# Kernel optimization log

Hardware: AMD Instinct MI355X
Metric: run time of the kernel (lower is better)

The kernel has to match this reference:

```python
import jax, jax.numpy as jnp
import numpy as np

NEG_SLOPE = 0.01  # LeakyReLU default
STRIDE = 5        # group_length // 4
EPS = 1e-5        # RMSNorm eps


def leaky_relu(x):
    return jnp.where(x >= 0, x, NEG_SLOPE * x)


def rmsnorm(x, w):
    return x * jax.lax.rsqrt(jnp.mean(x * x, axis=-1, keepdims=True) + EPS) * w


def s6(x, fc1_w, fc1_b, fc2_w, fc2_b, fc3_w, fc3_b, A):
    # x: [B, L, D] with D = 2*d_model; A: [D, N]
    delta = jax.nn.softplus(x @ fc1_w.T + fc1_b)        # [B, L, D]
    Bm = x @ fc2_w.T + fc2_b                             # [B, L, N]
    Cm = x @ fc3_w.T + fc3_b                             # [B, L, N]
    dA = jnp.exp(jnp.einsum('bld,dn->bldn', delta, A))   # [B, L, D, N]
    dBx = jnp.einsum('bld,bln,bld->bldn', delta, Bm, x)  # delta * B * x

    def step(h, inp):
        dA_t, dBx_t = inp
        h = dA_t * h + dBx_t
        return h, h

    B_, L, D, N = dA.shape
    h0 = jnp.zeros((B_, D, N), dtype=x.dtype)
    _, hs = jax.lax.scan(step, h0, (jnp.swapaxes(dA, 0, 1), jnp.swapaxes(dBx, 0, 1)))
    hs = jnp.swapaxes(hs, 0, 1)                          # [B, L, D, N]
    return jnp.einsum('bln,bldn->bld', Cm, hs)           # [B, L, D]


def setup_inputs() -> dict:
    key = jax.random.key(0)
    ks = iter(jax.random.split(key, 32))

    def rn(shape, scale=0.02):
        return scale * jax.random.normal(next(ks), shape, dtype=jnp.float32)

    B, band, gl, d, N, L = 256, 189, 20, 128, 128, 34
    di = 2 * d
    return {
        'x': jax.random.normal(next(ks), (B, 1, band), dtype=jnp.float32),
        'conv_w': rn((d, 1, gl)), 'conv_b': rn((d,)),
        'norm_w': jnp.ones((d,), jnp.float32),
        'inp_w': rn((di, d)), 'inp_b': rn((di,)),
        'seqconv_w': rn((L, L, 3)), 'seqconv_b': rn((L,)),
        'convlin_w': rn((di, di)), 'convlin_b': rn((di,)),
        'fc1_w': rn((di, di)), 'fc1_b': rn((di,)),
        'fc2_w': rn((N, di)), 'fc2_b': rn((N,)),
        'fc3_w': rn((N, di)), 'fc3_b': rn((N,)),
        'A': jnp.ones((di, N), jnp.float32) / jnp.sqrt(jnp.float32(N)),
        'D_w': rn((di, d)), 'D_b': rn((di,)),
        'out_w': rn((d, di)), 'out_b': rn((d,)),
        'fnn1_w': rn((64, L * d)), 'fnn1_b': rn((64,)),
        'fnn2_w': rn((32, 64)), 'fnn2_b': rn((32,)),
    }


def reference(x, conv_w, conv_b, norm_w, inp_w, inp_b, seqconv_w, seqconv_b,
              convlin_w, convlin_b, fc1_w, fc1_b, fc2_w, fc2_b, fc3_w, fc3_b,
              A, D_w, D_b, out_w, out_b, fnn1_w, fnn1_b, fnn2_w, fnn2_b):
    # group division: Conv1d(1, d, k=20, stride=5) + LeakyReLU
    g = jax.lax.conv_general_dilated(x, conv_w, (STRIDE,), [(0, 0)],
                                     dimension_numbers=('NCH', 'OIH', 'NCH'))
    g = leaky_relu(g + conv_b[None, :, None])            # [B, d, L]
    h = jnp.swapaxes(g, 1, 2)                            # [B, L, d]
    # Mamba block
    xn = rmsnorm(h, norm_w)
    xp = xn @ inp_w.T + inp_b                            # [B, L, 2d]
    # Conv1d(seq_len, seq_len, k=3, pad=1): seq axis L is the channel dim
    xc = jax.lax.conv_general_dilated(xp, seqconv_w, (1,), [(1, 1)],
                                      dimension_numbers=('NCH', 'OIH', 'NCH'))
    xc = jax.nn.silu(xc + seqconv_b[None, :, None])
    xc = xc @ convlin_w.T + convlin_b                    # [B, L, 2d]
    xs = s6(xc, fc1_w, fc1_b, fc2_w, fc2_b, fc3_w, fc3_b, A)
    y = jax.nn.silu(xs) * jax.nn.silu(xn @ D_w.T + D_b)  # gated
    y = y @ out_w.T + out_b                              # [B, L, d]
    # FNN head
    f = y.reshape(y.shape[0], -1)                        # [B, L*d]
    f = leaky_relu(f @ fnn1_w.T + fnn1_b)
    return f @ fnn2_w.T + fnn2_b                         # [B, 32]
```

## Files before the change

### kernel.cpp

```cpp
#include <hip/hip_runtime.h>
#include <math.h>


#define NB    256
#define LL    34
#define DD    128
#define DI    256
#define NN    128
#define MM    (NB*LL)

using u16 = unsigned short;
typedef __attribute__((ext_vector_type(8))) short short8;
typedef __attribute__((ext_vector_type(4))) float f32x4;

__device__ __forceinline__ float silu_f(float x)  { return x / (1.f + __expf(-x)); }
__device__ __forceinline__ float softplus_f(float x) {
    return fmaxf(x, 0.f) + __logf(1.f + __expf(-fabsf(x)));
}
__device__ __forceinline__ float leaky_f(float x) { return (x >= 0.f) ? x : 0.01f * x; }

__device__ __forceinline__ u16 f2bf(float x) {
    unsigned u = __float_as_uint(x);
    return (u16)((u + 0x7FFF + ((u >> 16) & 1)) >> 16);
}
__device__ __forceinline__ float bf2f(u16 h) {
    return __uint_as_float(((unsigned)h) << 16);
}
__device__ __forceinline__ void f2pair(float v, u16* h, u16* l) {
    u16 hh = f2bf(v);
    *h = hh;
    *l = f2bf(v - bf2f(hh));
}

__global__ __launch_bounds__(256)
void prep_all_k(const float* __restrict__ inp_w, const float* __restrict__ D_w,
                const float* __restrict__ fc1_w, const float* __restrict__ fc2_w,
                const float* __restrict__ fc3_w, const float* __restrict__ convlin_w,
                const float* __restrict__ out_w,
                const float* __restrict__ inp_b, const float* __restrict__ D_b,
                const float* __restrict__ fc1_b, const float* __restrict__ fc2_b,
                const float* __restrict__ fc3_b,
                const float* __restrict__ W1, const float* __restrict__ A,
                u16* __restrict__ wc1h, u16* __restrict__ wc1l,
                u16* __restrict__ wc3h, u16* __restrict__ wc3l,
                u16* __restrict__ cvh,  u16* __restrict__ cvl,
                u16* __restrict__ owh,  u16* __restrict__ owl,
                float* __restrict__ bias1, float* __restrict__ bias3,
                float* __restrict__ W1T, int* __restrict__ flag)
{
    const int bx  = blockIdx.x;
    const int tid = threadIdx.x;
    __shared__ float tile[64][65];

    if (bx < 1152) {
        int i = bx * 256 + tid;
        if (i < 65536) {
            float v = (i < 32768) ? inp_w[i] : D_w[i - 32768];
            f2pair(v, &wc1h[i], &wc1l[i]);
        } else if (i < 196608) {
            int j = i - 65536;
            float v = (j < 65536) ? fc1_w[j] : (j < 98304 ? fc2_w[j - 65536] : fc3_w[j - 98304]);
            f2pair(v, &wc3h[j], &wc3l[j]);
        } else if (i < 262144) {
            int j = i - 196608;
            f2pair(convlin_w[j], &cvh[j], &cvl[j]);
        } else if (i < 294912) {
            int j = i - 262144;
            f2pair(out_w[j], &owh[j], &owl[j]);
        }
        if (i < 512)  bias1[i] = (i < 256) ? inp_b[i] : D_b[i - 256];
        else if (i < 1024) {
            int j = i - 512;
            bias3[j] = (j < 256) ? fc1_b[j] : (j < 384 ? fc2_b[j - 256] : fc3_b[j - 384]);
        }
    } else if (bx < 1220) {
        const int bt = bx - 1152;
        for (int p = 0; p < 16; p++) {
            int idx = tid + p * 256;
            int r = idx >> 6, c = idx & 63;
            tile[r][c] = W1[(size_t)r * 4352 + bt * 64 + c];
        }
        __syncthreads();
        for (int p = 0; p < 16; p++) {
            int idx = tid + p * 256;
            int cc = idx >> 6, rr = idx & 63;
            W1T[(size_t)(bt * 64 + cc) * 64 + rr] = tile[rr][cc];
        }
    } else {
        __shared__ int s;
        if (tid == 0) s = 1;
        __syncthreads();
        bool ok = true;
        for (int k = 0; k < 128; k++) {
            int idx = tid + k * 256;
            ok &= (A[idx] == A[idx & ~127]);
        }
        if (!ok) s = 0;
        __syncthreads();
        if (tid == 0) *flag = s;
    }
}

__global__ __launch_bounds__(128)
void conv_norm_k(const float* __restrict__ x, const float* __restrict__ cw,
                 const float* __restrict__ cb, const float* __restrict__ nw,
                 u16* __restrict__ XNh, u16* __restrict__ XNl)
{
    int bl = blockIdx.x;
    int b = bl / LL, l = bl % LL;
    int c = threadIdx.x;
    const float* xr = x + (size_t)b * 189 + l * 5;
    float g = cb[c];
    #pragma unroll
    for (int k = 0; k < 20; k++) g = fmaf(xr[k], cw[c * 20 + k], g);
    g = leaky_f(g);

    float s = g * g;
    #pragma unroll
    for (int m = 32; m >= 1; m >>= 1) s += __shfl_xor(s, m);
    __shared__ float wsum[2];
    if ((threadIdx.x & 63) == 0) wsum[threadIdx.x >> 6] = s;
    __syncthreads();
    float mean = (wsum[0] + wsum[1]) * (1.f / 128.f);
    float inv = 1.f / sqrtf(mean + 1e-5f);
    float v = g * inv * nw[c];
    f2pair(v, &XNh[(size_t)bl * DD + c], &XNl[(size_t)bl * DD + c]);
}

template <int K, int EPI>
__global__ __launch_bounds__(256)
void mgemm_k(const u16* __restrict__ Ah, const u16* __restrict__ Al,
             const u16* __restrict__ Wh, const u16* __restrict__ Wl,
             const float* __restrict__ bias,
             float* __restrict__ Y, int ldy,
             u16* __restrict__ Yh, u16* __restrict__ Yl,
             u16* __restrict__ BC)
{
    const int tid  = threadIdx.x;
    const int r0   = blockIdx.x * 128;
    const int c0   = blockIdx.y * 64;
    const int wave = tid >> 6;
    const int lane = tid & 63;
    const int wm   = wave & 1;
    const int wn   = wave >> 1;
    const int l15  = lane & 15;
    const int lq   = lane >> 4;

    __shared__ u16 sAh[128][40];
    __shared__ u16 sAl[128][40];
    __shared__ u16 sBh[64][40];
    __shared__ u16 sBl[64][40];

    f32x4 acc[4][2];
    #pragma unroll
    for (int i = 0; i < 4; i++)
        #pragma unroll
        for (int j = 0; j < 2; j++) acc[i][j] = (f32x4){0.f, 0.f, 0.f, 0.f};

    const int a_row = tid >> 1;
    const int a_kb  = (tid & 1) * 16;
    const int b_row = tid >> 2;
    const int b_ko  = (tid & 3) * 8;

    for (int k0 = 0; k0 < K; k0 += 32) {
        const u16* ga = Ah + (size_t)(r0 + a_row) * K + k0 + a_kb;
        const u16* gl = Al + (size_t)(r0 + a_row) * K + k0 + a_kb;
        short8 vh0 = *(const short8*)(ga);
        short8 vh1 = *(const short8*)(ga + 8);
        short8 vl0 = *(const short8*)(gl);
        short8 vl1 = *(const short8*)(gl + 8);
        const u16* gb = Wh + (size_t)(c0 + b_row) * K + k0 + b_ko;
        const u16* gc = Wl + (size_t)(c0 + b_row) * K + k0 + b_ko;
        short8 wb = *(const short8*)(gb);
        short8 wc = *(const short8*)(gc);

        *(short8*)&sAh[a_row][a_kb]     = vh0;
        *(short8*)&sAh[a_row][a_kb + 8] = vh1;
        *(short8*)&sAl[a_row][a_kb]     = vl0;
        *(short8*)&sAl[a_row][a_kb + 8] = vl1;
        *(short8*)&sBh[b_row][b_ko] = wb;
        *(short8*)&sBl[b_row][b_ko] = wc;
        __syncthreads();

        short8 fah[4], fal[4], fbh[2], fbl[2];
        #pragma unroll
        for (int i = 0; i < 4; i++) {
            fah[i] = *(const short8*)&sAh[wm * 64 + i * 16 + l15][lq * 8];
            fal[i] = *(const short8*)&sAl[wm * 64 + i * 16 + l15][lq * 8];
        }
        #pragma unroll
        for (int j = 0; j < 2; j++) {
            fbh[j] = *(const short8*)&sBh[wn * 32 + j * 16 + l15][lq * 8];
            fbl[j] = *(const short8*)&sBl[wn * 32 + j * 16 + l15][lq * 8];
        }
        #pragma unroll
        for (int i = 0; i < 4; i++)
            #pragma unroll
            for (int j = 0; j < 2; j++) {
                acc[i][j] = __builtin_amdgcn_mfma_f32_16x16x32_bf16(fah[i], fbh[j], acc[i][j], 0, 0, 0);
                acc[i][j] = __builtin_amdgcn_mfma_f32_16x16x32_bf16(fah[i], fbl[j], acc[i][j], 0, 0, 0);
                acc[i][j] = __builtin_amdgcn_mfma_f32_16x16x32_bf16(fal[i], fbh[j], acc[i][j], 0, 0, 0);
            }
        __syncthreads();
    }

    #pragma unroll
    for (int i = 0; i < 4; i++) {
        int gr = r0 + wm * 64 + i * 16 + lq * 4;
        #pragma unroll
        for (int j = 0; j < 2; j++) {
            int gc = c0 + wn * 32 + j * 16 + l15;
            float bb = bias[gc];
            #pragma unroll
            for (int r = 0; r < 4; r++) {
                float v = acc[i][j][r] + bb;
                if (EPI == 1 || EPI == 3) { if (gc < 256) v = softplus_f(v); }
                if (EPI == 2) {
                    u16 hh, ll;
                    f2pair(v, &hh, &ll);
                    Yh[(size_t)(gr + r) * ldy + gc] = hh;
                    Yl[(size_t)(gr + r) * ldy + gc] = ll;
                } else {
                    Y[(size_t)(gr + r) * ldy + gc] = v;
                    if (EPI == 3 && gc >= 256) {
                        u16 hh, ll;
                        f2pair(v, &hh, &ll);
                        u16* rb = BC + (size_t)(gr + r) * 1024
                                     + ((gc < 384) ? 0 : 256) + (gc & 127);
                        rb[0]   = hh;
                        rb[128] = ll;
                    }
                }
            }
        }
    }
}

__global__ __launch_bounds__(256)
void seqconv_k(const float* __restrict__ XP, int ldxp,
               const float* __restrict__ w, const float* __restrict__ bias,
               u16* __restrict__ XCh, u16* __restrict__ XCl)
{
    const int b   = blockIdx.x;
    const int tid = threadIdx.x;
    const int tx  = tid & 63;
    const int ty  = tid >> 6;
    const int j0  = tx * 4;

    __shared__ float sx[LL][264];
    __shared__ float sw[LL][112];

    for (int idx = tid; idx < LL * 256; idx += 256) {
        int li = idx >> 8, jj = idx & 255;
        sx[li][jj + 1] = XP[(size_t)(b * LL + li) * ldxp + jj];
    }
    if (tid < LL) { sx[tid][0] = 0.f; sx[tid][257] = 0.f; }
    for (int idx = tid; idx < LL * LL * 3; idx += 256) {
        int lo = idx / 102;
        int rem = idx - lo * 102;
        int li = rem / 3;
        int k  = rem - li * 3;
        sw[li][lo * 3 + k] = w[idx];
    }
    __syncthreads();

    const int base = ty * 9 - (ty == 3 ? 1 : 0);
    const int cnt  = (ty < 2) ? 9 : 8;

    float acc[9][4];
    #pragma unroll
    for (int i = 0; i < 9; i++)
        #pragma unroll
        for (int jj = 0; jj < 4; jj++) acc[i][jj] = 0.f;

    for (int li = 0; li < LL; li++) {
        float4 xa = *(const float4*)&sx[li][j0];
        float2 xb = *(const float2*)&sx[li][j0 + 4];
        float xv[6] = {xa.x, xa.y, xa.z, xa.w, xb.x, xb.y};
        const float* swr = &sw[li][0];
        #pragma unroll
        for (int i = 0; i < 9; i++) {
            if (i < cnt) {
                int lo3 = (base + i) * 3;
                float w0 = swr[lo3 + 0];
                float w1 = swr[lo3 + 1];
                float w2 = swr[lo3 + 2];
                #pragma unroll
                for (int jj = 0; jj < 4; jj++) {
                    acc[i][jj] = fmaf(w0, xv[jj],     acc[i][jj]);
                    acc[i][jj] = fmaf(w1, xv[jj + 1], acc[i][jj]);
                    acc[i][jj] = fmaf(w2, xv[jj + 2], acc[i][jj]);
                }
            }
        }
    }

    #pragma unroll
    for (int i = 0; i < 9; i++) {
        if (i < cnt) {
            int lo = base + i;
            float bb = bias[lo];
            ushort4 oh, ol;
            float v0 = silu_f(acc[i][0] + bb);
            float v1 = silu_f(acc[i][1] + bb);
            float v2 = silu_f(acc[i][2] + bb);
            float v3 = silu_f(acc[i][3] + bb);
            f2pair(v0, &oh.x, &ol.x);
            f2pair(v1, &oh.y, &ol.y);
            f2pair(v2, &oh.z, &ol.z);
            f2pair(v3, &oh.w, &ol.w);
            size_t o = (size_t)(b * LL + lo) * DI + j0;
            *(ushort4*)&XCh[o] = oh;
            *(ushort4*)&XCl[o] = ol;
        }
    }
}

__global__ __launch_bounds__(256)
void ssd_scan_k(const int* __restrict__ flag,
                const float* __restrict__ dBC,
                const u16* __restrict__ BC,
                const u16* __restrict__ Xh, const u16* __restrict__ Xl,
                const float* __restrict__ A,
                const float* __restrict__ DG,
                u16* __restrict__ Gh, u16* __restrict__ Gl)
{
    if (*flag == 0) return;
    const int b    = blockIdx.x;
    const int tid  = threadIdx.x;
    const int wave = tid >> 6;
    const int lane = tid & 63;
    const int l15  = lane & 15;
    const int lq   = lane >> 4;

    __shared__ u16 sBh[48][136], sBl[48][136];
    __shared__ u16 sCh[48][136], sCl[48][136];
    __shared__ float sM[48][49];

    const u16* base = BC + (size_t)b * LL * 1024;
    for (int idx = tid; idx < LL * 16; idx += 256) {
        int l = idx >> 4, c = (idx & 15) << 3;
        const u16* row = base + l * 1024;
        *(short8*)&sBh[l][c] = *(const short8*)&row[c];
        *(short8*)&sBl[l][c] = *(const short8*)&row[128 + c];
        *(short8*)&sCh[l][c] = *(const short8*)&row[256 + c];
        *(short8*)&sCl[l][c] = *(const short8*)&row[384 + c];
    }
    __syncthreads();

    for (int tt = wave; tt < 9; tt += 4) {
        int ti = tt / 3, tj = tt - ti * 3;
        f32x4 acc = (f32x4){0.f, 0.f, 0.f, 0.f};
        #pragma unroll
        for (int ks = 0; ks < 4; ks++) {
            short8 ch = *(const short8*)&sCh[ti * 16 + l15][ks * 32 + lq * 8];
            short8 cl = *(const short8*)&sCl[ti * 16 + l15][ks * 32 + lq * 8];
            short8 bh = *(const short8*)&sBh[tj * 16 + l15][ks * 32 + lq * 8];
            short8 bl = *(const short8*)&sBl[tj * 16 + l15][ks * 32 + lq * 8];
            acc = __builtin_amdgcn_mfma_f32_16x16x32_bf16(ch, bh, acc, 0, 0, 0);
            acc = __builtin_amdgcn_mfma_f32_16x16x32_bf16(ch, bl, acc, 0, 0, 0);
            acc = __builtin_amdgcn_mfma_f32_16x16x32_bf16(cl, bh, acc, 0, 0, 0);
        }
        #pragma unroll
        for (int r = 0; r < 4; r++)
            sM[ti * 16 + lq * 4 + r][tj * 16 + l15] = acc[r];
    }
    __syncthreads();

    const int d = tid;
    const float a_d = A[(size_t)d * NN];
    const float* pDel = dBC + (size_t)b * LL * 512 + d;
    const u16* pXh = Xh + (size_t)b * LL * 256 + d;
    const u16* pXl = Xl + (size_t)b * LL * 256 + d;

    float u[LL], eS[LL];
    float S = 0.f;
    #pragma unroll
    for (int l = 0; l < LL; l++) {
        float dl = pDel[l * 512];
        S = fmaf(dl, a_d, S);
        eS[l] = __expf(S);
        float xv = bf2f(pXh[l * 256]) + bf2f(pXl[l * 256]);
        u[l] = __expf(-S) * dl * xv;
    }

    const float* pG = DG + (size_t)b * LL * 512 + 256 + d;
    u16* pGh = Gh + (size_t)b * LL * 256 + d;
    u16* pGl = Gl + (size_t)b * LL * 256 + d;
    #pragma unroll
    for (int l = 0; l < LL; l++) {
        float acc = 0.f;
        for (int t = 0; t <= l; t++) acc = fmaf(sM[l][t], u[t], acc);
        float xs = eS[l] * acc;
        float g = silu_f(xs) * silu_f(pG[l * 512]);
        u16 hh, ll2;
        f2pair(g, &hh, &ll2);
        pGh[l * 256] = hh;
        pGl[l * 256] = ll2;
    }
}

__global__ __launch_bounds__(256)
void scan_fb_k(const int* __restrict__ flag,
               const float* __restrict__ dBC,
               const u16*  __restrict__ Xh, const u16* __restrict__ Xl,
               const float* __restrict__ A,
               const float* __restrict__ DG,
               u16* __restrict__ Gh, u16* __restrict__ Gl)
{
    if (*flag != 0) return;
    const int b  = blockIdx.y;
    const int d0 = blockIdx.x * 64;
    const int tid = threadIdx.x;
    const int sub = tid & 15;
    const int pg  = tid >> 4;
    const int dbase = d0 + pg * 4;
    const int nA = sub * 4;

    float a[4][8], h[4][8];
    #pragma unroll
    for (int dd = 0; dd < 4; dd++) {
        const float* Ar = A + (size_t)(dbase + dd) * NN;
        float4 q0 = *(const float4*)(Ar + nA);
        float4 q1 = *(const float4*)(Ar + 64 + nA);
        a[dd][0]=q0.x; a[dd][1]=q0.y; a[dd][2]=q0.z; a[dd][3]=q0.w;
        a[dd][4]=q1.x; a[dd][5]=q1.y; a[dd][6]=q1.z; a[dd][7]=q1.w;
        #pragma unroll
        for (int j = 0; j < 8; j++) h[dd][j] = 0.f;
    }

    const float* pD  = dBC + (size_t)b * LL * 512 + dbase;
    const float* pBC = dBC + (size_t)b * LL * 512 + 256 + nA;
    const u16*  pXh = Xh  + (size_t)b * LL * 256 + dbase;
    const u16*  pXl = Xl  + (size_t)b * LL * 256 + dbase;
    const float* pG  = DG  + (size_t)b * LL * 512 + 256 + dbase;
    u16* pGh = Gh + (size_t)b * LL * 256 + dbase;
    u16* pGl = Gl + (size_t)b * LL * 256 + dbase;

    for (int l = 0; l < LL; l++) {
        float4  cD  = *(const float4*)(pD);
        ushort4 cXh = *(const ushort4*)(pXh);
        ushort4 cXl = *(const ushort4*)(pXl);
        float4 cB0 = *(const float4*)(pBC);
        float4 cB1 = *(const float4*)(pBC + 64);
        float4 cC0 = *(const float4*)(pBC + 128);
        float4 cC1 = *(const float4*)(pBC + 192);
        pD += 512; pBC += 512; pXh += 256; pXl += 256;

        float xv[4] = { bf2f(cXh.x) + bf2f(cXl.x), bf2f(cXh.y) + bf2f(cXl.y),
                        bf2f(cXh.z) + bf2f(cXl.z), bf2f(cXh.w) + bf2f(cXl.w) };
        float dl[4] = {cD.x, cD.y, cD.z, cD.w};
        float dx[4] = {cD.x * xv[0], cD.y * xv[1], cD.z * xv[2], cD.w * xv[3]};
        float bv[8] = {cB0.x,cB0.y,cB0.z,cB0.w,cB1.x,cB1.y,cB1.z,cB1.w};
        float cv[8] = {cC0.x,cC0.y,cC0.z,cC0.w,cC1.x,cC1.y,cC1.z,cC1.w};

        float accd[4] = {0.f, 0.f, 0.f, 0.f};
        #pragma unroll
        for (int dd = 0; dd < 4; dd++)
            #pragma unroll
            for (int j = 0; j < 8; j++) {
                float dA = __expf(dl[dd] * a[dd][j]);
                h[dd][j] = fmaf(dA, h[dd][j], dx[dd] * bv[j]);
                accd[dd] = fmaf(cv[j], h[dd][j], accd[dd]);
            }
        #pragma unroll
        for (int dd = 0; dd < 4; dd++) {
            float v = accd[dd];
            v += __shfl_xor(v, 1);
            v += __shfl_xor(v, 2);
            v += __shfl_xor(v, 4);
            v += __shfl_xor(v, 8);
            accd[dd] = v;
        }
        if (sub == 0) {
            float4 dg = *(const float4*)(pG);
            ushort4 oh, ol;
            float g0 = silu_f(accd[0]) * silu_f(dg.x);
            float g1 = silu_f(accd[1]) * silu_f(dg.y);
            float g2 = silu_f(accd[2]) * silu_f(dg.z);
            float g3 = silu_f(accd[3]) * silu_f(dg.w);
            f2pair(g0, &oh.x, &ol.x);
            f2pair(g1, &oh.y, &ol.y);
            f2pair(g2, &oh.z, &ol.z);
            f2pair(g3, &oh.w, &ol.w);
            *(ushort4*)pGh = oh;
            *(ushort4*)pGl = ol;
        }
        pG += 512; pGh += 256; pGl += 256;
    }
}

__global__ __launch_bounds__(256)
void fnn1_k(const float* __restrict__ F, const float* __restrict__ W1T,
            float* __restrict__ partials)
{
    const int btile = blockIdx.x;
    const int kc    = blockIdx.y;
    const int tid   = threadIdx.x;
    __shared__ float sf[16][260];
    for (int i = tid; i < 16 * 256; i += 256) {
        int r = i >> 8, c = i & 255;
        sf[r][c] = F[(size_t)(btile * 16 + r) * 4352 + kc * 256 + c];
    }
    __syncthreads();

    const int o  = tid & 63;
    const int bq = tid >> 6;
    const float* w = W1T + (size_t)(kc * 256) * 64 + o;
    float acc[4] = {0.f, 0.f, 0.f, 0.f};
    for (int k = 0; k < 256; k += 4) {
        float w0 = w[(size_t)(k + 0) * 64];
        float w1 = w[(size_t)(k + 1) * 64];
        float w2 = w[(size_t)(k + 2) * 64];
        float w3 = w[(size_t)(k + 3) * 64];
        #pragma unroll
        for (int bj = 0; bj < 4; bj++) {
            float4 f4 = *(const float4*)&sf[bq * 4 + bj][k];
            acc[bj] = fmaf(w0, f4.x, acc[bj]);
            acc[bj] = fmaf(w1, f4.y, acc[bj]);
            acc[bj] = fmaf(w2, f4.z, acc[bj]);
            acc[bj] = fmaf(w3, f4.w, acc[bj]);
        }
    }
    #pragma unroll
    for (int bj = 0; bj < 4; bj++)
        partials[(size_t)kc * 16384 + (btile * 16 + bq * 4 + bj) * 64 + o] = acc[bj];
}

__global__ __launch_bounds__(64)
void fnn2_k(const float* __restrict__ partials,
            const float* __restrict__ B1,
            const float* __restrict__ W2, const float* __restrict__ B2,
            float* __restrict__ out)
{
    int b = blockIdx.x;
    int t = threadIdx.x;
    __shared__ float s1[64];
    float acc = B1[t];
    #pragma unroll
    for (int kc = 0; kc < 17; kc++)
        acc += partials[(size_t)kc * 16384 + b * 64 + t];
    s1[t] = leaky_f(acc);
    __syncthreads();

    if (t < 32) {
        float acc2 = B2[t];
        const float* w2 = W2 + t * 64;
        #pragma unroll
        for (int j = 0; j < 64; j++) acc2 = fmaf(s1[j], w2[j], acc2);
        out[(size_t)b * 32 + t] = acc2;
    }
}

extern "C" void kernel_launch(void* const* d_in, const int* in_sizes, int n_in,
                              void* d_out, int out_size, void* d_ws, size_t ws_size,
                              hipStream_t stream)
{
    const float* x        = (const float*)d_in[0];
    const float* conv_w   = (const float*)d_in[1];
    const float* conv_b   = (const float*)d_in[2];
    const float* norm_w   = (const float*)d_in[3];
    const float* inp_w    = (const float*)d_in[4];
    const float* inp_b    = (const float*)d_in[5];
    const float* seqconv_w= (const float*)d_in[6];
    const float* seqconv_b= (const float*)d_in[7];
    const float* convlin_w= (const float*)d_in[8];
    const float* convlin_b= (const float*)d_in[9];
    const float* fc1_w    = (const float*)d_in[10];
    const float* fc1_b    = (const float*)d_in[11];
    const float* fc2_w    = (const float*)d_in[12];
    const float* fc2_b    = (const float*)d_in[13];
    const float* fc3_w    = (const float*)d_in[14];
    const float* fc3_b    = (const float*)d_in[15];
    const float* A        = (const float*)d_in[16];
    const float* D_w      = (const float*)d_in[17];
    const float* D_b      = (const float*)d_in[18];
    const float* out_w    = (const float*)d_in[19];
    const float* out_b    = (const float*)d_in[20];
    const float* fnn1_w   = (const float*)d_in[21];
    const float* fnn1_b   = (const float*)d_in[22];
    const float* fnn2_w   = (const float*)d_in[23];
    const float* fnn2_b   = (const float*)d_in[24];

    char* W = (char*)d_ws;
    float* buf1  = (float*)(W + 0);
    float* buf3  = (float*)(W + 17825792);
    u16*   xnh   = (u16*)  (W + 35651584);
    u16*   xnl   = (u16*)  (W + 37879808);
    u16*   xc2h  = (u16*)  (W + 35651584);
    float* fout  = (float*)(W + 35651584);
    u16*   xc2l  = (u16*)  (W + 40108032);
    u16*   xch   = (u16*)  (W + 44564480);
    u16*   xcl   = (u16*)  (W + 49020928);
    float* w1t   = (float*)(W + 53477376);
    u16*   wc1h  = (u16*)  (W + 54591488);
    u16*   wc1l  = (u16*)  (W + 54722560);
    u16*   wc3h  = (u16*)  (W + 54853632);
    u16*   wc3l  = (u16*)  (W + 55115776);
    u16*   cvh   = (u16*)  (W + 55377920);
    u16*   cvl   = (u16*)  (W + 55508992);
    u16*   owh   = (u16*)  (W + 55640064);
    u16*   owl   = (u16*)  (W + 55705600);
    float* bias1 = (float*)(W + 55771136);
    float* bias3 = (float*)(W + 55773184);
    int*   uflag = (int*)  (W + 55775232);
    u16* gateh = xch;
    u16* gatel = xcl;
    u16* bcpair = (u16*)buf1;
    float* partials = buf3;

    prep_all_k<<<1221, 256, 0, stream>>>(inp_w, D_w, fc1_w, fc2_w, fc3_w,
                                         convlin_w, out_w,
                                         inp_b, D_b, fc1_b, fc2_b, fc3_b,
                                         fnn1_w, A,
                                         wc1h, wc1l, wc3h, wc3l, cvh, cvl,
                                         owh, owl, bias1, bias3, w1t, uflag);

    conv_norm_k<<<MM, 128, 0, stream>>>(x, conv_w, conv_b, norm_w, xnh, xnl);

    mgemm_k<128, 0><<<dim3(MM / 128, 8), 256, 0, stream>>>(
        xnh, xnl, wc1h, wc1l, bias1, buf1, 512, nullptr, nullptr, nullptr);

    seqconv_k<<<NB, 256, 0, stream>>>(buf1, 512, seqconv_w, seqconv_b, xch, xcl);

    mgemm_k<256, 2><<<dim3(MM / 128, 4), 256, 0, stream>>>(
        xch, xcl, cvh, cvl, convlin_b, nullptr, 256, xc2h, xc2l, nullptr);

    mgemm_k<256, 3><<<dim3(MM / 128, 8), 256, 0, stream>>>(
        xc2h, xc2l, wc3h, wc3l, bias3, buf3, 512, nullptr, nullptr, bcpair);

    ssd_scan_k<<<NB, 256, 0, stream>>>(uflag, buf3, bcpair, xc2h, xc2l, A,
                                       buf1, gateh, gatel);
    scan_fb_k<<<dim3(4, NB), 256, 0, stream>>>(uflag, buf3, xc2h, xc2l, A,
                                               buf1, gateh, gatel);

    mgemm_k<256, 0><<<dim3(MM / 128, 2), 256, 0, stream>>>(
        gateh, gatel, owh, owl, out_b, fout, 128, nullptr, nullptr, nullptr);

    fnn1_k<<<dim3(16, 17), 256, 0, stream>>>(fout, w1t, partials);
    fnn2_k<<<NB, 64, 0, stream>>>(partials, fnn1_b, fnn2_w, fnn2_b,
                                  (float*)d_out);
}
```

Before: 220.5 us.

## Fuse conv+norm into prep, widen GEMM N-tile, merge scan kernels

Folds the conv+RMSNorm stage into the prep kernel as extra blocks, each handling two rows, so one launch is removed. The GEMM gains a BN template parameter, and three GEMMs now use 128-wide column tiles, which doubles A-tile reuse at the cost of more accumulator registers. The two scan kernels are merged into one flag-dispatched kernel. Its SSD path now splits across 4 d-blocks per batch and 4 waves per block, and each wave handles an interleaved subset of timesteps with a fully unrolled triangular inner loop. The merged path recomputes the BC matrix product in each of the 4 blocks per batch.

After: 226.4 us. +2.7%, slower.

```diff
diff --git a/kernel.cpp b/kernel.cpp
--- a/kernel.cpp
+++ b/kernel.cpp
@@ -41,16 +41,21 @@
                 const float* __restrict__ fc1_b, const float* __restrict__ fc2_b,
                 const float* __restrict__ fc3_b,
                 const float* __restrict__ W1, const float* __restrict__ A,
+                const float* __restrict__ xin, const float* __restrict__ cw,
+                const float* __restrict__ cb, const float* __restrict__ nw,
                 u16* __restrict__ wc1h, u16* __restrict__ wc1l,
                 u16* __restrict__ wc3h, u16* __restrict__ wc3l,
                 u16* __restrict__ cvh,  u16* __restrict__ cvl,
                 u16* __restrict__ owh,  u16* __restrict__ owl,
                 float* __restrict__ bias1, float* __restrict__ bias3,
-                float* __restrict__ W1T, int* __restrict__ flag)
+                float* __restrict__ W1T, int* __restrict__ flag,
+                u16* __restrict__ XNh, u16* __restrict__ XNl)
 {
     const int bx  = blockIdx.x;
     const int tid = threadIdx.x;
     __shared__ float tile[64][65];
+    __shared__ float wsum[4];
+    __shared__ int sflag;
 
     if (bx < 1152) {
         int i = bx * 256 + tid;
@@ -86,48 +91,40 @@
             int cc = idx >> 6, rr = idx & 63;
             W1T[(size_t)(bt * 64 + cc) * 64 + rr] = tile[rr][cc];
         }
-    } else {
-        __shared__ int s;
-        if (tid == 0) s = 1;
+    } else if (bx == 1220) {
+        if (tid == 0) sflag = 1;
         __syncthreads();
         bool ok = true;
         for (int k = 0; k < 128; k++) {
             int idx = tid + k * 256;
             ok &= (A[idx] == A[idx & ~127]);
         }
-        if (!ok) s = 0;
-        __syncthreads();
-        if (tid == 0) *flag = s;
-    }
-}
-
-__global__ __launch_bounds__(128)
-void conv_norm_k(const float* __restrict__ x, const float* __restrict__ cw,
-                 const float* __restrict__ cb, const float* __restrict__ nw,
-                 u16* __restrict__ XNh, u16* __restrict__ XNl)
-{
-    int bl = blockIdx.x;
-    int b = bl / LL, l = bl % LL;
-    int c = threadIdx.x;
-    const float* xr = x + (size_t)b * 189 + l * 5;
-    float g = cb[c];
-    #pragma unroll
-    for (int k = 0; k < 20; k++) g = fmaf(xr[k], cw[c * 20 + k], g);
-    g = leaky_f(g);
-
-    float s = g * g;
-    #pragma unroll
-    for (int m = 32; m >= 1; m >>= 1) s += __shfl_xor(s, m);
-    __shared__ float wsum[2];
-    if ((threadIdx.x & 63) == 0) wsum[threadIdx.x >> 6] = s;
-    __syncthreads();
-    float mean = (wsum[0] + wsum[1]) * (1.f / 128.f);
-    float inv = 1.f / sqrtf(mean + 1e-5f);
-    float v = g * inv * nw[c];
-    f2pair(v, &XNh[(size_t)bl * DD + c], &XNl[(size_t)bl * DD + c]);
-}
-
-template <int K, int EPI>
+        if (!ok) sflag = 0;
+        __syncthreads();
+        if (tid == 0) *flag = sflag;
+    } else {
+        const int half = tid >> 7;
+        const int c    = tid & 127;
+        const int bl   = (bx - 1221) * 2 + half;
+        const int b = bl / LL, l = bl % LL;
+        const float* xr = xin + (size_t)b * 189 + l * 5;
+        float g = cb[c];
+        #pragma unroll
+        for (int k = 0; k < 20; k++) g = fmaf(xr[k], cw[c * 20 + k], g);
+        g = leaky_f(g);
+        float s = g * g;
+        #pragma unroll
+        for (int m = 32; m >= 1; m >>= 1) s += __shfl_xor(s, m);
+        if ((tid & 63) == 0) wsum[tid >> 6] = s;
+        __syncthreads();
+        float mean = (wsum[half * 2] + wsum[half * 2 + 1]) * (1.f / 128.f);
+        float inv = 1.f / sqrtf(mean + 1e-5f);
+        float v = g * inv * nw[c];
+        f2pair(v, &XNh[(size_t)bl * DD + c], &XNl[(size_t)bl * DD + c]);
+    }
+}
+
+template <int K, int BN, int EPI>
 __global__ __launch_bounds__(256)
 void mgemm_k(const u16* __restrict__ Ah, const u16* __restrict__ Al,
              const u16* __restrict__ Wh, const u16* __restrict__ Wl,
@@ -136,9 +133,10 @@
              u16* __restrict__ Yh, u16* __restrict__ Yl,
              u16* __restrict__ BC)
 {
+    constexpr int JT = BN / 32;
     const int tid  = threadIdx.x;
     const int r0   = blockIdx.x * 128;
-    const int c0   = blockIdx.y * 64;
+    const int c0   = blockIdx.y * BN;
     const int wave = tid >> 6;
     const int lane = tid & 63;
     const int wm   = wave & 1;
@@ -148,19 +146,19 @@
 
     __shared__ u16 sAh[128][40];
     __shared__ u16 sAl[128][40];
-    __shared__ u16 sBh[64][40];
-    __shared__ u16 sBl[64][40];
-
-    f32x4 acc[4][2];
+    __shared__ u16 sBh[BN][40];
+    __shared__ u16 sBl[BN][40];
+
+    f32x4 acc[4][JT];
     #pragma unroll
     for (int i = 0; i < 4; i++)
         #pragma unroll
-        for (int j = 0; j < 2; j++) acc[i][j] = (f32x4){0.f, 0.f, 0.f, 0.f};
+        for (int j = 0; j < JT; j++) acc[i][j] = (f32x4){0.f, 0.f, 0.f, 0.f};
 
     const int a_row = tid >> 1;
     const int a_kb  = (tid & 1) * 16;
-    const int b_row = tid >> 2;
-    const int b_ko  = (tid & 3) * 8;
+    const int b_row = (BN == 128) ? (tid >> 1) : (tid >> 2);
+    const int b_ko  = (BN == 128) ? ((tid & 1) * 16) : ((tid & 3) * 8);
 
     for (int k0 = 0; k0 < K; k0 += 32) {
         const u16* ga = Ah + (size_t)(r0 + a_row) * K + k0 + a_kb;
@@ -171,32 +169,41 @@
         short8 vl1 = *(const short8*)(gl + 8);
         const u16* gb = Wh + (size_t)(c0 + b_row) * K + k0 + b_ko;
         const u16* gc = Wl + (size_t)(c0 + b_row) * K + k0 + b_ko;
-        short8 wb = *(const short8*)(gb);
-        short8 wc = *(const short8*)(gc);
+        short8 wb0 = *(const short8*)(gb);
+        short8 wc0 = *(const short8*)(gc);
+        short8 wb1, wc1;
+        if (BN == 128) {
+            wb1 = *(const short8*)(gb + 8);
+            wc1 = *(const short8*)(gc + 8);
+        }
 
         *(short8*)&sAh[a_row][a_kb]     = vh0;
         *(short8*)&sAh[a_row][a_kb + 8] = vh1;
         *(short8*)&sAl[a_row][a_kb]     = vl0;
         *(short8*)&sAl[a_row][a_kb + 8] = vl1;
-        *(short8*)&sBh[b_row][b_ko] = wb;
-        *(short8*)&sBl[b_row][b_ko] = wc;
-        __syncthreads();
-
-        short8 fah[4], fal[4], fbh[2], fbl[2];
+        *(short8*)&sBh[b_row][b_ko] = wb0;
+        *(short8*)&sBl[b_row][b_ko] = wc0;
+        if (BN == 128) {
+            *(short8*)&sBh[b_row][b_ko + 8] = wb1;
+            *(short8*)&sBl[b_row][b_ko + 8] = wc1;
+        }
+        __syncthreads();
+
+        short8 fah[4], fal[4], fbh[JT], fbl[JT];
         #pragma unroll
         for (int i = 0; i < 4; i++) {
             fah[i] = *(const short8*)&sAh[wm * 64 + i * 16 + l15][lq * 8];
             fal[i] = *(const short8*)&sAl[wm * 64 + i * 16 + l15][lq * 8];
         }
         #pragma unroll
-        for (int j = 0; j < 2; j++) {
-            fbh[j] = *(const short8*)&sBh[wn * 32 + j * 16 + l15][lq * 8];
-            fbl[j] = *(const short8*)&sBl[wn * 32 + j * 16 + l15][lq * 8];
+        for (int j = 0; j < JT; j++) {
+            fbh[j] = *(const short8*)&sBh[wn * (BN / 2) + j * 16 + l15][lq * 8];
+            fbl[j] = *(const short8*)&sBl[wn * (BN / 2) + j * 16 + l15][lq * 8];
         }
         #pragma unroll
         for (int i = 0; i < 4; i++)
             #pragma unroll
-            for (int j = 0; j < 2; j++) {
+            for (int j = 0; j < JT; j++) {
                 acc[i][j] = __builtin_amdgcn_mfma_f32_16x16x32_bf16(fah[i], fbh[j], acc[i][j], 0, 0, 0);
                 acc[i][j] = __builtin_amdgcn_mfma_f32_16x16x32_bf16(fah[i], fbl[j], acc[i][j], 0, 0, 0);
                 acc[i][j] = __builtin_amdgcn_mfma_f32_16x16x32_bf16(fal[i], fbh[j], acc[i][j], 0, 0, 0);
@@ -208,8 +215,8 @@
     for (int i = 0; i < 4; i++) {
         int gr = r0 + wm * 64 + i * 16 + lq * 4;
         #pragma unroll
-        for (int j = 0; j < 2; j++) {
-            int gc = c0 + wn * 32 + j * 16 + l15;
+        for (int j = 0; j < JT; j++) {
+            int gc = c0 + wn * (BN / 2) + j * 16 + l15;
             float bb = bias[gc];
             #pragma unroll
             for (int r = 0; r < 4; r++) {
@@ -316,81 +323,17 @@
     }
 }
 
-__global__ __launch_bounds__(256)
-void ssd_scan_k(const int* __restrict__ flag,
-                const float* __restrict__ dBC,
-                const u16* __restrict__ BC,
-                const u16* __restrict__ Xh, const u16* __restrict__ Xl,
-                const float* __restrict__ A,
-                const float* __restrict__ DG,
-                u16* __restrict__ Gh, u16* __restrict__ Gl)
-{
-    if (*flag == 0) return;
-    const int b    = blockIdx.x;
-    const int tid  = threadIdx.x;
-    const int wave = tid >> 6;
-    const int lane = tid & 63;
-    const int l15  = lane & 15;
-    const int lq   = lane >> 4;
-
-    __shared__ u16 sBh[48][136], sBl[48][136];
-    __shared__ u16 sCh[48][136], sCl[48][136];
-    __shared__ float sM[48][49];
-
-    const u16* base = BC + (size_t)b * LL * 1024;
-    for (int idx = tid; idx < LL * 16; idx += 256) {
-        int l = idx >> 4, c = (idx & 15) << 3;
-        const u16* row = base + l * 1024;
-        *(short8*)&sBh[l][c] = *(const short8*)&row[c];
-        *(short8*)&sBl[l][c] = *(const short8*)&row[128 + c];
-        *(short8*)&sCh[l][c] = *(const short8*)&row[256 + c];
-        *(short8*)&sCl[l][c] = *(const short8*)&row[384 + c];
-    }
-    __syncthreads();
-
-    for (int tt = wave; tt < 9; tt += 4) {
-        int ti = tt / 3, tj = tt - ti * 3;
-        f32x4 acc = (f32x4){0.f, 0.f, 0.f, 0.f};
-        #pragma unroll
-        for (int ks = 0; ks < 4; ks++) {
-            short8 ch = *(const short8*)&sCh[ti * 16 + l15][ks * 32 + lq * 8];
-            short8 cl = *(const short8*)&sCl[ti * 16 + l15][ks * 32 + lq * 8];
-            short8 bh = *(const short8*)&sBh[tj * 16 + l15][ks * 32 + lq * 8];
-            short8 bl = *(const short8*)&sBl[tj * 16 + l15][ks * 32 + lq * 8];
-            acc = __builtin_amdgcn_mfma_f32_16x16x32_bf16(ch, bh, acc, 0, 0, 0);
-            acc = __builtin_amdgcn_mfma_f32_16x16x32_bf16(ch, bl, acc, 0, 0, 0);
-            acc = __builtin_amdgcn_mfma_f32_16x16x32_bf16(cl, bh, acc, 0, 0, 0);
-        }
-        #pragma unroll
-        for (int r = 0; r < 4; r++)
-            sM[ti * 16 + lq * 4 + r][tj * 16 + l15] = acc[r];
-    }
-    __syncthreads();
-
-    const int d = tid;
-    const float a_d = A[(size_t)d * NN];
-    const float* pDel = dBC + (size_t)b * LL * 512 + d;
-    const u16* pXh = Xh + (size_t)b * LL * 256 + d;
-    const u16* pXl = Xl + (size_t)b * LL * 256 + d;
-
-    float u[LL], eS[LL];
-    float S = 0.f;
-    #pragma unroll
-    for (int l = 0; l < LL; l++) {
-        float dl = pDel[l * 512];
-        S = fmaf(dl, a_d, S);
-        eS[l] = __expf(S);
-        float xv = bf2f(pXh[l * 256]) + bf2f(pXl[l * 256]);
-        u[l] = __expf(-S) * dl * xv;
-    }
-
-    const float* pG = DG + (size_t)b * LL * 512 + 256 + d;
-    u16* pGh = Gh + (size_t)b * LL * 256 + d;
-    u16* pGl = Gl + (size_t)b * LL * 256 + d;
-    #pragma unroll
-    for (int l = 0; l < LL; l++) {
+template <int Q>
+__device__ __forceinline__ void ssd_tail(const float (*Msh)[49],
+                                         const float (&u)[LL], const float (&eS)[LL],
+                                         const float* __restrict__ pG,
+                                         u16* __restrict__ pGh, u16* __restrict__ pGl)
+{
+    #pragma unroll
+    for (int l = Q; l < LL; l += 4) {
         float acc = 0.f;
-        for (int t = 0; t <= l; t++) acc = fmaf(sM[l][t], u[t], acc);
+        #pragma unroll
+        for (int t = 0; t <= l; t++) acc = fmaf(Msh[l][t], u[t], acc);
         float xs = eS[l] * acc;
         float g = silu_f(xs) * silu_f(pG[l * 512]);
         u16 hh, ll2;
@@ -401,17 +344,89 @@
 }
 
 __global__ __launch_bounds__(256)
-void scan_fb_k(const int* __restrict__ flag,
-               const float* __restrict__ dBC,
-               const u16*  __restrict__ Xh, const u16* __restrict__ Xl,
-               const float* __restrict__ A,
-               const float* __restrict__ DG,
-               u16* __restrict__ Gh, u16* __restrict__ Gl)
-{
-    if (*flag != 0) return;
-    const int b  = blockIdx.y;
-    const int d0 = blockIdx.x * 64;
+void scan_k(const int* __restrict__ flag,
+            const float* __restrict__ dBC,
+            const u16* __restrict__ BC,
+            const u16* __restrict__ Xh, const u16* __restrict__ Xl,
+            const float* __restrict__ A,
+            const float* __restrict__ DG,
+            u16* __restrict__ Gh, u16* __restrict__ Gl)
+{
+    const int bx  = blockIdx.x;
+    const int b   = blockIdx.y;
     const int tid = threadIdx.x;
+
+    __shared__ u16 sBh[48][136], sBl[48][136];
+    __shared__ u16 sCh[48][136], sCl[48][136];
+    __shared__ float sM[48][49];
+
+    if (*flag != 0) {
+        const int wave = tid >> 6;
+        const int lane = tid & 63;
+        const int l15  = lane & 15;
+        const int lq   = lane >> 4;
+
+        const u16* base = BC + (size_t)b * LL * 1024;
+        for (int idx = tid; idx < LL * 16; idx += 256) {
+            int l = idx >> 4, c = (idx & 15) << 3;
+            const u16* row = base + l * 1024;
+            *(short8*)&sBh[l][c] = *(const short8*)&row[c];
+            *(short8*)&sBl[l][c] = *(const short8*)&row[128 + c];
+            *(short8*)&sCh[l][c] = *(const short8*)&row[256 + c];
+            *(short8*)&sCl[l][c] = *(const short8*)&row[384 + c];
+        }
+        __syncthreads();
+
+        for (int tt = wave; tt < 9; tt += 4) {
+            int ti = tt / 3, tj = tt - ti * 3;
+            f32x4 acc = (f32x4){0.f, 0.f, 0.f, 0.f};
+            #pragma unroll
+            for (int ks = 0; ks < 4; ks++) {
+                short8 ch = *(const short8*)&sCh[ti * 16 + l15][ks * 32 + lq * 8];
+                short8 cl = *(const short8*)&sCl[ti * 16 + l15][ks * 32 + lq * 8];
+                short8 bh = *(const short8*)&sBh[tj * 16 + l15][ks * 32 + lq * 8];
+                short8 bl = *(const short8*)&sBl[tj * 16 + l15][ks * 32 + lq * 8];
+                acc = __builtin_amdgcn_mfma_f32_16x16x32_bf16(ch, bh, acc, 0, 0, 0);
+                acc = __builtin_amdgcn_mfma_f32_16x16x32_bf16(ch, bl, acc, 0, 0, 0);
+                acc = __builtin_amdgcn_mfma_f32_16x16x32_bf16(cl, bh, acc, 0, 0, 0);
+            }
+            #pragma unroll
+            for (int r = 0; r < 4; r++)
+                sM[ti * 16 + lq * 4 + r][tj * 16 + l15] = acc[r];
+        }
+        __syncthreads();
+
+        const int d = (bx << 6) + lane;
+        const int q = wave;
+        const float a_d = A[(size_t)d * NN];
+        const float* pDel = dBC + (size_t)b * LL * 512 + d;
+        const u16* pXh = Xh + (size_t)b * LL * 256 + d;
+        const u16* pXl = Xl + (size_t)b * LL * 256 + d;
+
+        float u[LL], eS[LL];
+        float S = 0.f;
+        #pragma unroll
+        for (int l = 0; l < LL; l++) {
+            float dl = pDel[l * 512];
+            S = fmaf(dl, a_d, S);
+            eS[l] = __expf(S);
+            float xv = bf2f(pXh[l * 256]) + bf2f(pXl[l * 256]);
+            u[l] = __expf(-S) * dl * xv;
+        }
+
+        const float* pG = DG + (size_t)b * LL * 512 + 256 + d;
+        u16* pGh = Gh + (size_t)b * LL * 256 + d;
+        u16* pGl = Gl + (size_t)b * LL * 256 + d;
+        switch (q) {
+            case 0: ssd_tail<0>(sM, u, eS, pG, pGh, pGl); break;
+            case 1: ssd_tail<1>(sM, u, eS, pG, pGh, pGl); break;
+            case 2: ssd_tail<2>(sM, u, eS, pG, pGh, pGl); break;
+            default: ssd_tail<3>(sM, u, eS, pG, pGh, pGl); break;
+        }
+        return;
+    }
+
+    const int d0 = bx * 64;
     const int sub = tid & 15;
     const int pg  = tid >> 4;
     const int dbase = d0 + pg * 4;
@@ -609,32 +624,29 @@
     u16* bcpair = (u16*)buf1;
     float* partials = buf3;
 
-    prep_all_k<<<1221, 256, 0, stream>>>(inp_w, D_w, fc1_w, fc2_w, fc3_w,
+    prep_all_k<<<5573, 256, 0, stream>>>(inp_w, D_w, fc1_w, fc2_w, fc3_w,
                                          convlin_w, out_w,
                                          inp_b, D_b, fc1_b, fc2_b, fc3_b,
-                                         fnn1_w, A,
+                                         fnn1_w, A, x, conv_w, conv_b, norm_w,
                                          wc1h, wc1l, wc3h, wc3l, cvh, cvl,
-                                         owh, owl, bias1, bias3, w1t, uflag);
-
-    conv_norm_k<<<MM, 128, 0, stream>>>(x, conv_w, conv_b, norm_w, xnh, xnl);
-
-    mgemm_k<128, 0><<<dim3(MM / 128, 8), 256, 0, stream>>>(
+                                         owh, owl, bias1, bias3, w1t, uflag,
+                                         xnh, xnl);
+
+    mgemm_k<128, 128, 0><<<dim3(MM / 128, 4), 256, 0, stream>>>(
         xnh, xnl, wc1h, wc1l, bias1, buf1, 512, nullptr, nullptr, nullptr);
 
     seqconv_k<<<NB, 256, 0, stream>>>(buf1, 512, seqconv_w, seqconv_b, xch, xcl);
 
-    mgemm_k<256, 2><<<dim3(MM / 128, 4), 256, 0, stream>>>(
+    mgemm_k<256, 128, 2><<<dim3(MM / 128, 2), 256, 0, stream>>>(
         xch, xcl, cvh, cvl, convlin_b, nullptr, 256, xc2h, xc2l, nullptr);
 
-    mgemm_k<256, 3><<<dim3(MM / 128, 8), 256, 0, stream>>>(
+    mgemm_k<256, 128, 3><<<dim3(MM / 128, 4), 256, 0, stream>>>(
         xc2h, xc2l, wc3h, wc3l, bias3, buf3, 512, nullptr, nullptr, bcpair);
 
-    ssd_scan_k<<<NB, 256, 0, stream>>>(uflag, buf3, bcpair, xc2h, xc2l, A,
-                                       buf1, gateh, gatel);
-    scan_fb_k<<<dim3(4, NB), 256, 0, stream>>>(uflag, buf3, xc2h, xc2l, A,
-                                               buf1, gateh, gatel);
-
-    mgemm_k<256, 0><<<dim3(MM / 128, 2), 256, 0, stream>>>(
+    scan_k<<<dim3(4, NB), 256, 0, stream>>>(uflag, buf3, bcpair, xc2h, xc2l,
+                                            A, buf1, gateh, gatel);
+
+    mgemm_k<256, 64, 0><<<dim3(MM / 128, 2), 256, 0, stream>>>(
         gateh, gatel, owh, owl, out_b, fout, 128, nullptr, nullptr, nullptr);
 
     fnn1_k<<<dim3(16, 17), 256, 0, stream>>>(fout, w1t, partials);
```
